# Kernel tuning notes

Measured on AMD Instinct MI355X. Metric: run time of the kernel, lower is better.

The kernel has to match this reference:

```python
import jax, jax.numpy as jnp
import numpy as np

NUM_SAMPLES = 512
FG_FRACTION = 0.25
MAX_POS = int(NUM_SAMPLES * FG_FRACTION)  # 128
THRESHOLDS = np.array([0.0, 0.5, 0.5], dtype=np.float32)
INDICATORS = np.array([-3, -1, -2, 1], dtype=np.int32)


def _make_boxes(key, shape, scale):
    # random valid boxes: sorted corner pairs in [0, scale)
    y = jnp.sort(jax.random.uniform(key, shape[:-1] + (2,)) * scale, axis=-1)
    x = jnp.sort(jax.random.uniform(jax.random.fold_in(key, 1), shape[:-1] + (2,)) * scale, axis=-1)
    return jnp.stack([y[..., 0], x[..., 0], y[..., 1], x[..., 1]], axis=-1)


def setup_inputs() -> dict:
    key = jax.random.key(0)
    k1, k2, k3, k4 = jax.random.split(key, 4)
    B, N, M = 32, 8000, 256
    boxes = _make_boxes(k1, (B, N, 4), 1024.0)
    gt_boxes = _make_boxes(k2, (B, M, 4), 1024.0)
    # pad last quarter of gt entries with -1 (invalid)
    valid = (jnp.arange(M) < (3 * M) // 4)[None, :, None]
    gt_boxes = jnp.where(valid, gt_boxes, -jnp.ones_like(gt_boxes))
    gt_classes = jax.random.randint(k3, (B, M), 1, 91, dtype=jnp.int32)
    gt_classes = jnp.where(valid[..., 0], gt_classes, -1)
    rand = jax.random.uniform(k4, (B, N + M))
    return {"boxes": boxes, "gt_boxes": gt_boxes, "gt_classes": gt_classes, "rand": rand}


def _pairwise_iou(b1, b2):
    # b1: [B,N,4], b2: [B,M,4] in (ymin,xmin,ymax,xmax) -> [B,N,M]
    ymin1, xmin1, ymax1, xmax1 = jnp.split(b1, 4, axis=-1)  # each [B,N,1]
    ymin2, xmin2, ymax2, xmax2 = (t[..., 0] for t in jnp.split(b2, 4, axis=-1))  # [B,M]
    ih = jnp.clip(jnp.minimum(ymax1, ymax2[:, None, :]) - jnp.maximum(ymin1, ymin2[:, None, :]), 0.0)
    iw = jnp.clip(jnp.minimum(xmax1, xmax2[:, None, :]) - jnp.maximum(xmin1, xmin2[:, None, :]), 0.0)
    inter = ih * iw
    a1 = (ymax1 - ymin1) * (xmax1 - xmin1)          # [B,N,1]
    a2 = (ymax2 - ymin2) * (xmax2 - xmin2)          # [B,M]
    union = a1 + a2[:, None, :] - inter
    return jnp.where(union > 0, inter / union, 0.0)


def _ranks_desc(score):
    order = jnp.argsort(-score)
    return jnp.zeros_like(order).at[order].set(jnp.arange(score.shape[0]))


def _sample_one(pos, neg, ign, rand):
    cand = (pos | neg) & ~ign
    pos_c = pos & cand
    neg_c = neg & cand
    pos_rank = _ranks_desc(jnp.where(pos_c, rand, -1.0))
    pos_sel = pos_c & (pos_rank < MAX_POS)
    neg_needed = NUM_SAMPLES - jnp.sum(pos_sel)
    neg_rank = _ranks_desc(jnp.where(neg_c, rand, -1.0))
    neg_sel = neg_c & (neg_rank < neg_needed)
    indicator = (pos_sel | neg_sel).astype(jnp.int32)
    _, idx = jax.lax.top_k(indicator, NUM_SAMPLES)  # selected first, ties by lowest index
    return idx


def _gather(t, idx):
    # t: [B,L,C], idx: [B,K] -> [B,K,C]
    return jnp.take_along_axis(t, idx[..., None], axis=1)


def reference(boxes, gt_boxes, gt_classes, rand):
    gt_boxes = gt_boxes.astype(boxes.dtype)
    boxes = jnp.concatenate([boxes, gt_boxes], axis=1)  # mix_gt_boxes
    boxes_invalid = jnp.max(boxes, axis=-1) < 0.0       # [B,L]
    gt_invalid = jnp.max(gt_boxes, axis=-1) < 0.0       # [B,M]
    sim = _pairwise_iou(boxes, gt_boxes)                # [B,L,M]
    sim = jnp.where(boxes_invalid[:, :, None] | gt_invalid[:, None, :], -1.0, sim)

    matched_vals = jnp.max(sim, axis=-1)                # [B,L]
    matched_gt_indices = jnp.argmax(sim, axis=-1).astype(jnp.int32)
    bucket = jnp.searchsorted(jnp.asarray(THRESHOLDS), matched_vals, side='right')
    match_indicators = jnp.asarray(INDICATORS)[bucket]  # [B,L]

    positive = match_indicators >= 0
    negative = match_indicators == -1
    ignored = match_indicators == -2
    invalid = match_indicators == -3
    background = negative | invalid                     # [B,L]

    matched_gt_classes = _gather(gt_classes[..., None], matched_gt_indices)[..., 0]
    matched_gt_classes = jnp.where(background, 0, matched_gt_classes)
    matched_gt_boxes = _gather(gt_boxes, matched_gt_indices)
    matched_gt_boxes = jnp.where(background[..., None], 0.0, matched_gt_boxes)
    matched_gt_indices = jnp.where(background, -1, matched_gt_indices)

    indices = jax.vmap(_sample_one)(positive, negative, ignored, rand)  # [B,K]
    rois = _gather(boxes, indices)
    sampled_gt_boxes = _gather(matched_gt_boxes, indices)
    sampled_gt_classes = _gather(matched_gt_classes[..., None], indices)[..., 0]
    sampled_gt_indices = _gather(matched_gt_indices[..., None], indices)[..., 0]
    return rois, sampled_gt_boxes, sampled_gt_classes, sampled_gt_indices
```

## Files before the change

kernel.cpp:

```cpp
#include <hip/hip_runtime.h>
#include <stdint.h>

#define BB 32
#define NN 8000
#define MM 256
#define LL (NN + MM)
#define NSAMP 512
#define MAXPOS 128
#define T2 1024
#define CH ((LL + T2 - 1) / T2)
#define SPLIT 4
#define MSUB (MM / SPLIT)

__device__ __forceinline__ void opaquef(float& x) { asm("" : "+v"(x)); }

__device__ __noinline__ int serial_argmax(const float4 bx, const float a1,
                                          const float4* s_gt, const float* s_a2)
{
    float qb = -1.0f; int bi = 0;
    for (int m = 0; m < MSUB; ++m) {
        float4 g = s_gt[m];
        float ih = fmaxf(fminf(bx.z, g.z) - fmaxf(bx.x, g.x), 0.0f);
        float iw = fmaxf(fminf(bx.w, g.w) - fmaxf(bx.y, g.y), 0.0f);
        float inter = ih * iw; opaquef(inter);
        float uni = (a1 + s_a2[m]) - inter;
        float q = (uni > 0.0f) ? (inter / uni) : 0.0f;
        if (q > qb) { qb = q; bi = m; }
    }
    return bi;
}

__device__ __forceinline__ uint32_t approx_key(const float4 bx, float a1,
                                               const float4 g, float a2, int m)
{
    float ih = fmaxf(fminf(bx.z, g.z) - fmaxf(bx.x, g.x), 0.0f);
    float iw = fmaxf(fminf(bx.w, g.w) - fmaxf(bx.y, g.y), 0.0f);
    float inter = ih * iw;
    float s = fmaxf(a1 + a2, 1e-30f);
    float u = inter * __builtin_amdgcn_rcpf(s);
    return (__float_as_uint(u) & 0xFFFFFFC0u) | (uint32_t)(63 - m);
}

template<bool FUSED>
__global__ __launch_bounds__(256) void match_split_kernel(
    const float* __restrict__ boxes, const float* __restrict__ gt,
    void* __restrict__ outp)
{
    __shared__ float4 s_gt[MSUB];
    __shared__ float  s_a2[MSUB];
    const int b = blockIdx.y, sp = blockIdx.z, tid = threadIdx.x;
    if (tid < MSUB) {
        float4 v = ((const float4*)(gt + ((size_t)b * MM + sp * MSUB) * 4))[tid];
        s_gt[tid] = v;
        s_a2[tid] = (v.z - v.x) * (v.w - v.y);
    }
    __syncthreads();
    const int l0 = blockIdx.x * 512 + tid * 2;
    if (l0 >= LL) return;
    const int l1 = l0 + 1;
    const bool v1 = (l1 < LL);
    const int l1c = v1 ? l1 : l0;

    const float4* bb4 = (const float4*)(boxes + (size_t)b * NN * 4);
    const float4* gb4 = (const float4*)(gt + (size_t)b * MM * 4);
    float4 bx0 = (l0 < NN) ? bb4[l0] : gb4[l0 - NN];
    float4 bx1 = (l1c < NN) ? bb4[l1c] : gb4[l1c - NN];
    float a10 = (bx0.z - bx0.x) * (bx0.w - bx0.y); opaquef(a10);
    float a11 = (bx1.z - bx1.x) * (bx1.w - bx1.y); opaquef(a11);

    uint32_t best0 = 0, sec0 = 0, best1 = 0, sec1 = 0;
    #pragma unroll 8
    for (int m = 0; m < MSUB; ++m) {
        const float4 g = s_gt[m];
        const float a2 = s_a2[m];
        {
            uint32_t key = approx_key(bx0, a10, g, a2, m);
            uint32_t old = best0;
            best0 = max(old, key);
            sec0  = max(sec0, min(old, key));
        }
        {
            uint32_t key = approx_key(bx1, a11, g, a2, m);
            uint32_t old = best1;
            best1 = max(old, key);
            sec1  = max(sec1, min(old, key));
        }
    }

    bool redo0 = ((best0 & ~63u) != 0u) &&
                 (((best0 & ~63u) - (sec0 & ~63u)) <= 64u);
    bool redo1 = v1 && ((best1 & ~63u) != 0u) &&
                 (((best1 & ~63u) - (sec1 & ~63u)) <= 64u);
    if (__any(redo0 || redo1)) {
        if (redo0) {
            int mW = serial_argmax(bx0, a10, s_gt, s_a2);
            best0 = approx_key(bx0, a10, s_gt[mW], s_a2[mW], mW);
        }
        if (redo1) {
            int mW = serial_argmax(bx1, a11, s_gt, s_a2);
            best1 = approx_key(bx1, a11, s_gt[mW], s_a2[mW], mW);
        }
    }
    if (FUSED) {
        uint32_t* keys = (uint32_t*)outp;
        keys[((size_t)b * LL + l0) * SPLIT + sp] = best0;
        if (v1) keys[((size_t)b * LL + l1) * SPLIT + sp] = best1;
    } else {
        uint8_t* pidx = (uint8_t*)outp;
        pidx[((size_t)b * LL + l0) * SPLIT + sp] = (uint8_t)(63 - (best0 & 63u));
        if (v1) pidx[((size_t)b * LL + l1) * SPLIT + sp] = (uint8_t)(63 - (best1 & 63u));
    }
}

__global__ __launch_bounds__(256) void merge_kernel(
    const float* __restrict__ boxes, const float* __restrict__ gt,
    const uint8_t* __restrict__ pidx, uint16_t* __restrict__ packed)
{
    const int b = blockIdx.y;
    const int l = blockIdx.x * 256 + threadIdx.x;
    if (l >= LL) return;
    float4 bx = (l < NN) ? ((const float4*)(boxes + (size_t)b * NN * 4))[l]
                         : ((const float4*)(gt + (size_t)b * MM * 4))[l - NN];
    int cls, bidx = 0;
    if (fmaxf(fmaxf(bx.x, bx.y), fmaxf(bx.z, bx.w)) < 0.0f) {
        cls = 2;
    } else {
        float a1 = (bx.z - bx.x) * (bx.w - bx.y); opaquef(a1);
        float qb = -1.0f;
        const uint32_t pv = *(const uint32_t*)&pidx[((size_t)b * LL + l) * SPLIT];
        #pragma unroll
        for (int sp = 0; sp < SPLIT; ++sp) {
            const int m = sp * MSUB + (int)((pv >> (8 * sp)) & 0xFFu);
            float4 g = ((const float4*)(gt + (size_t)b * MM * 4))[m];
            float a2 = (g.z - g.x) * (g.w - g.y); opaquef(a2);
            float ih = fmaxf(fminf(bx.z, g.z) - fmaxf(bx.x, g.x), 0.0f);
            float iw = fmaxf(fminf(bx.w, g.w) - fmaxf(bx.y, g.y), 0.0f);
            float inter = ih * iw; opaquef(inter);
            float uni = (a1 + a2) - inter;
            float q = (uni > 0.0f) ? (inter / uni) : 0.0f;
            if (q > qb) { qb = q; bidx = m; }
        }
        cls = (qb >= 0.5f) ? 1 : 0;
    }
    packed[(size_t)b * LL + l] = (uint16_t)(cls | (bidx << 2));
}

__device__ __forceinline__ int block_exscan_fast(int v, int* wt, int tid)
{
    const int lane = tid & 63, w = tid >> 6;
    int x = v;
    #pragma unroll
    for (int off = 1; off < 64; off <<= 1) {
        int y = __shfl_up(x, off);
        if (lane >= off) x += y;
    }
    if (lane == 63) wt[w] = x;
    __syncthreads();
    if (tid < 64) {
        int t = (tid < 16) ? wt[tid] : 0;
        #pragma unroll
        for (int off = 1; off < 16; off <<= 1) {
            int y = __shfl_up(t, off);
            if (tid >= off) t += y;
        }
        if (tid < 16) wt[tid] = t;
    }
    __syncthreads();
    return ((w > 0) ? wt[w - 1] : 0) + x - v;
}

__device__ __forceinline__ int block_exscan_seg4(int v, int* wt, int tid)
{
    const int lane = tid & 63, w = tid >> 6;
    int x = v;
    #pragma unroll
    for (int off = 1; off < 64; off <<= 1) {
        int y = __shfl_up(x, off);
        if (lane >= off) x += y;
    }
    if (lane == 63) wt[w] = x;
    __syncthreads();
    if (tid < 16) {
        int t = wt[tid];
        #pragma unroll
        for (int off = 1; off < 4; off <<= 1) {
            int y = __shfl_up(t, off);
            if ((tid & 3) >= off) t += y;
        }
        wt[tid] = t;
    }
    __syncthreads();
    return (((w & 3) > 0) ? wt[w - 1] : 0) + x - v;
}

template<bool FUSED>
__global__ __launch_bounds__(T2) void sample_kernel(
    const float* __restrict__ boxes, const float* __restrict__ gt,
    const int* __restrict__ gtc, const float* __restrict__ rnd,
    const void* __restrict__ matchp, float* __restrict__ out)
{
    __shared__ uint32_t s_key[LL];
    __shared__ uint16_t s_pk[LL];
    __shared__ int s_hist[512];
    __shared__ int s_warp[16];
    __shared__ int s_idx[NSAMP];
    __shared__ int s_sb[8];
    const int b = blockIdx.x, tid = threadIdx.x, lane = tid & 63;
    const float4* bb4 = (const float4*)(boxes + (size_t)b * NN * 4);
    const float4* gb4 = (const float4*)(gt + (size_t)b * MM * 4);

    if (tid == 0) s_sb[0] = 0;
    __syncthreads();

    int loc = 0;
    for (int l = tid; l < LL; l += T2) {
        s_key[l] = __float_as_uint(rnd[(size_t)b * LL + l]);
        int cls, midx;
        if (FUSED) {
            const uint4 kv = ((const uint4*)matchp)[(size_t)b * LL + l];
            float4 bx = (l < NN) ? bb4[l] : gb4[l - NN];
            if (fmaxf(fmaxf(bx.x, bx.y), fmaxf(bx.z, bx.w)) < 0.0f) {
                cls = 2; midx = 0;
            } else {
                uint32_t best = kv.x; int bsp = 0;
                if (kv.y > best) { best = kv.y; bsp = 1; }
                if (kv.z > best) { best = kv.z; bsp = 2; }
                if (kv.w > best) { best = kv.w; bsp = 3; }
                const uint32_t bt = best & ~63u;
                const uint32_t s0 = (bsp == 0) ? 0u : (kv.x & ~63u);
                const uint32_t s1 = (bsp == 1) ? 0u : (kv.y & ~63u);
                const uint32_t s2 = (bsp == 2) ? 0u : (kv.z & ~63u);
                const uint32_t s3 = (bsp == 3) ? 0u : (kv.w & ~63u);
                const uint32_t sec = max(max(s0, s1), max(s2, s3));
                float a1 = (bx.z - bx.x) * (bx.w - bx.y); opaquef(a1);
                if ((bt != 0u) && (bt - sec) <= 64u) {
                    float qb = -1.0f; midx = 0;
                    #pragma unroll
                    for (int sp = 0; sp < SPLIT; ++sp) {
                        const uint32_t k = (sp == 0) ? kv.x : (sp == 1) ? kv.y
                                         : (sp == 2) ? kv.z : kv.w;
                        const int m = sp * MSUB + (63 - (int)(k & 63u));
                        float4 g = gb4[m];
                        float a2 = (g.z - g.x) * (g.w - g.y); opaquef(a2);
                        float ih = fmaxf(fminf(bx.z, g.z) - fmaxf(bx.x, g.x), 0.0f);
                        float iw = fmaxf(fminf(bx.w, g.w) - fmaxf(bx.y, g.y), 0.0f);
                        float inter = ih * iw; opaquef(inter);
                        float uni = (a1 + a2) - inter;
                        float q = (uni > 0.0f) ? (inter / uni) : 0.0f;
                        if (q > qb) { qb = q; midx = m; }
                    }
                    cls = (qb >= 0.5f) ? 1 : 0;
                } else {
                    midx = bsp * MSUB + (63 - (int)(best & 63u));
                    float4 g = gb4[midx];
                    float a2 = (g.z - g.x) * (g.w - g.y); opaquef(a2);
                    float ih = fmaxf(fminf(bx.z, g.z) - fmaxf(bx.x, g.x), 0.0f);
                    float iw = fmaxf(fminf(bx.w, g.w) - fmaxf(bx.y, g.y), 0.0f);
                    float inter = ih * iw; opaquef(inter);
                    float uni = (a1 + a2) - inter;
                    float q = (uni > 0.0f) ? (inter / uni) : 0.0f;
                    cls = (q >= 0.5f) ? 1 : 0;
                }
            }
        } else {
            const uint16_t p = ((const uint16_t*)matchp)[(size_t)b * LL + l];
            cls = p & 3; midx = (p >> 2) & 0xFF;
        }
        s_pk[l] = (uint16_t)(cls | (midx << 2));
        loc += (cls == 0) ? 1 : ((cls == 1) ? 0x10000 : 0);
    }
    #pragma unroll
    for (int off = 32; off; off >>= 1) loc += __shfl_xor(loc, off);
    if (lane == 0) atomicAdd(&s_sb[0], loc);
    __syncthreads();
    const int Nn = s_sb[0] & 0xFFFF, P = s_sb[0] >> 16;

    const int posK = (P < MAXPOS) ? P : MAXPOS;
    const int negK = NSAMP - posK;
    const bool negRad = (Nn > negK);
    const bool posRad = (P > MAXPOS);

    uint32_t prefix0 = 0, prefix1 = 0;
    int rem0 = negK, rem1 = MAXPOS;
    if (negRad || posRad) {
        for (int round = 0; round < 4; ++round) {
            const int shift = 24 - 8 * round;
            if (tid < 512) s_hist[tid] = 0;
            __syncthreads();
            const uint32_t pmask = (round == 0) ? 0u : (0xFFFFFFFFu << (shift + 8));
            for (int l = tid; l < LL; l += T2) {
                const uint32_t k = s_key[l];
                const int c = s_pk[l] & 3;
                bool doit = (c == 0) ? (negRad && ((k & pmask) == prefix0))
                          : (c == 1) ? (posRad && ((k & pmask) == prefix1))
                          : false;
                if (doit) atomicAdd(&s_hist[(c << 8) | ((k >> shift) & 255)], 1);
            }
            __syncthreads();
            int h = 0;
            if (tid < 512) h = s_hist[(tid & 0x100) | (255 - (tid & 255))];
            const int above = block_exscan_seg4(h, s_warp, tid);
            if (tid < 512) {
                const int c = tid >> 8;
                const int rem = c ? rem1 : rem0;
                const bool act = c ? posRad : negRad;
                if (act && above < rem && above + h >= rem) {
                    s_sb[4 + c * 2] = 255 - (tid & 255);
                    s_sb[5 + c * 2] = above;
                }
            }
            __syncthreads();
            if (negRad) { prefix0 |= ((uint32_t)s_sb[4]) << shift; rem0 -= s_sb[5]; }
            if (posRad) { prefix1 |= ((uint32_t)s_sb[6]) << shift; rem1 -= s_sb[7]; }
            __syncthreads();
        }
    }
    const uint32_t thr0 = negRad ? prefix0 : 0u;  const int r0 = negRad ? rem0 : LL;
    const uint32_t thr1 = posRad ? prefix1 : 0u;  const int r1 = posRad ? rem1 : LL;

    const int lo = tid * CH, hi = (lo + CH < LL) ? (lo + CH) : LL;
    int nt = 0;
    for (int l = lo; l < hi; ++l) {
        const int c = s_pk[l] & 3;
        const uint32_t k = s_key[l];
        if (c == 0) { if (k == thr0) nt += 1; }
        else if (c == 1) { if (k == thr1) nt += 0x10000; }
    }
    const int basep = block_exscan_fast(nt, s_warp, tid);
    int base0 = basep & 0xFFFF, base1 = basep >> 16;
    for (int l = lo; l < hi; ++l) {
        const int c = s_pk[l] & 3;
        if (c > 1) continue;
        const uint32_t k = s_key[l];
        const uint32_t thr = c ? thr1 : thr0;
        bool sel = (k > thr);
        if (k == thr) {
            if (c == 0) { sel = (base0 < r0); ++base0; }
            else        { sel = (base1 < r1); ++base1; }
        }
        if (sel) s_pk[l] |= 0x8000;
    }
    __syncthreads();

    int cnt = 0;
    for (int l = lo; l < hi; ++l) cnt += (s_pk[l] & 0x8000) ? 1 : 0x10000;
    const int pb = block_exscan_fast(cnt, s_warp, tid);
    const int S = s_warp[15] & 0xFFFF;
    int bs = pb & 0xFFFF, bu = (pb >> 16) + S;
    for (int l = lo; l < hi; ++l) {
        if (s_pk[l] & 0x8000) { if (bs < NSAMP) s_idx[bs] = l; ++bs; }
        else                  { if (bu < NSAMP) s_idx[bu] = l; ++bu; }
    }
    __syncthreads();

    if (tid < NSAMP) {
        const int l = s_idx[tid];
        float4 bx = (l < NN) ? bb4[l] : gb4[l - NN];
        const int p = s_pk[l];
        const int c = p & 3, mi = (p >> 2) & 0xFF;
        const bool bg = (c != 1);
        float4 gb = make_float4(0.f, 0.f, 0.f, 0.f);
        int cl = 0, si = -1;
        if (!bg) {
            gb = gb4[mi];
            cl = gtc[(size_t)b * MM + mi];
            si = mi;
        }
        const size_t rk = (size_t)b * NSAMP + tid;
        ((float4*)out)[rk] = bx;
        ((float4*)(out + (size_t)BB * NSAMP * 4))[rk] = gb;
        out[(size_t)2 * BB * NSAMP * 4 + rk] = (float)cl;
        out[(size_t)2 * BB * NSAMP * 4 + (size_t)BB * NSAMP + rk] = (float)si;
    }
}

extern "C" void kernel_launch(void* const* d_in, const int* in_sizes, int n_in,
                              void* d_out, int out_size, void* d_ws, size_t ws_size,
                              hipStream_t stream)
{
    const float* boxes = (const float*)d_in[0];
    const float* gt    = (const float*)d_in[1];
    const int*   gtc   = (const int*)  d_in[2];
    const float* rnd   = (const float*)d_in[3];
    float* out = (float*)d_out;

    dim3 g1((LL + 511) / 512, BB, SPLIT);
    const size_t need = (size_t)BB * LL * SPLIT * sizeof(uint32_t);
    if (ws_size >= need) {
        match_split_kernel<true><<<g1, 256, 0, stream>>>(boxes, gt, d_ws);
        sample_kernel<true><<<BB, T2, 0, stream>>>(boxes, gt, gtc, rnd, d_ws, out);
    } else {
        uint8_t*  pidx   = (uint8_t*)d_ws;
        uint16_t* packed = (uint16_t*)((char*)d_ws + (size_t)BB * LL * SPLIT);
        match_split_kernel<false><<<g1, 256, 0, stream>>>(boxes, gt, pidx);
        dim3 g2((LL + 255) / 256, BB);
        merge_kernel<<<g2, 256, 0, stream>>>(boxes, gt, pidx, packed);
        sample_kernel<false><<<BB, T2, 0, stream>>>(boxes, gt, gtc, rnd, packed, out);
    }
}
```

Measured before the change: 75.49 us.

## Compact invalid GT boxes out of match loop and split key merge into separate kernel

The match kernel now compacts each 64-wide GT slice in shared memory so that only valid (non-padded) GT boxes are scanned. It keeps the original index in a per-entry key suffix so tie-breaking is preserved. The 4-way key merge and exact IoU recheck move out of the 32-block sample kernel into a new wide merge kernel, which writes a packed class/index in place into the key buffer. This spreads the serial per-row merge work across many blocks but adds a third kernel launch and an extra global round trip.

Measured after the change: 70.97 us. -6.0%, faster.

```diff
diff --git a/kernel.cpp b/kernel.cpp
--- a/kernel.cpp
+++ b/kernel.cpp
@@ -14,11 +14,24 @@
 
 __device__ __forceinline__ void opaquef(float& x) { asm("" : "+v"(x)); }
 
+__device__ __forceinline__ uint32_t approx_key(const float4 bx, float a1,
+                                               const float4 g, float a2,
+                                               uint32_t klo)
+{
+    float ih = fmaxf(fminf(bx.z, g.z) - fmaxf(bx.x, g.x), 0.0f);
+    float iw = fmaxf(fminf(bx.w, g.w) - fmaxf(bx.y, g.y), 0.0f);
+    float inter = ih * iw;
+    float s = fmaxf(a1 + a2, 1e-30f);
+    float u = inter * __builtin_amdgcn_rcpf(s);
+    return (__float_as_uint(u) & 0xFFFFFFC0u) | klo;
+}
+
 __device__ __noinline__ int serial_argmax(const float4 bx, const float a1,
-                                          const float4* s_gt, const float* s_a2)
+                                          const float4* s_gt, const float* s_a2,
+                                          int nv)
 {
     float qb = -1.0f; int bi = 0;
-    for (int m = 0; m < MSUB; ++m) {
+    for (int m = 0; m < nv; ++m) {
         float4 g = s_gt[m];
         float ih = fmaxf(fminf(bx.z, g.z) - fmaxf(bx.x, g.x), 0.0f);
         float iw = fmaxf(fminf(bx.w, g.w) - fmaxf(bx.y, g.y), 0.0f);
@@ -30,29 +43,26 @@
     return bi;
 }
 
-__device__ __forceinline__ uint32_t approx_key(const float4 bx, float a1,
-                                               const float4 g, float a2, int m)
-{
-    float ih = fmaxf(fminf(bx.z, g.z) - fmaxf(bx.x, g.x), 0.0f);
-    float iw = fmaxf(fminf(bx.w, g.w) - fmaxf(bx.y, g.y), 0.0f);
-    float inter = ih * iw;
-    float s = fmaxf(a1 + a2, 1e-30f);
-    float u = inter * __builtin_amdgcn_rcpf(s);
-    return (__float_as_uint(u) & 0xFFFFFFC0u) | (uint32_t)(63 - m);
-}
-
-template<bool FUSED>
 __global__ __launch_bounds__(256) void match_split_kernel(
     const float* __restrict__ boxes, const float* __restrict__ gt,
-    void* __restrict__ outp)
+    uint32_t* __restrict__ keys)
 {
     __shared__ float4 s_gt[MSUB];
     __shared__ float  s_a2[MSUB];
+    __shared__ uint32_t s_klo[MSUB];
+    __shared__ int s_nv;
     const int b = blockIdx.y, sp = blockIdx.z, tid = threadIdx.x;
     if (tid < MSUB) {
         float4 v = ((const float4*)(gt + ((size_t)b * MM + sp * MSUB) * 4))[tid];
-        s_gt[tid] = v;
-        s_a2[tid] = (v.z - v.x) * (v.w - v.y);
+        bool valid = !(fmaxf(fmaxf(v.x, v.y), fmaxf(v.z, v.w)) < 0.0f);
+        uint64_t mk = __ballot(valid);
+        int pos = __popcll(mk & ((1ull << tid) - 1));
+        if (valid) {
+            s_gt[pos] = v;
+            s_a2[pos] = (v.z - v.x) * (v.w - v.y);
+            s_klo[pos] = (uint32_t)(63 - tid);
+        }
+        if (tid == 0) s_nv = (int)__popcll(mk);
     }
     __syncthreads();
     const int l0 = blockIdx.x * 512 + tid * 2;
@@ -60,6 +70,7 @@
     const int l1 = l0 + 1;
     const bool v1 = (l1 < LL);
     const int l1c = v1 ? l1 : l0;
+    const int nv = s_nv;
 
     const float4* bb4 = (const float4*)(boxes + (size_t)b * NN * 4);
     const float4* gb4 = (const float4*)(gt + (size_t)b * MM * 4);
@@ -69,18 +80,19 @@
     float a11 = (bx1.z - bx1.x) * (bx1.w - bx1.y); opaquef(a11);
 
     uint32_t best0 = 0, sec0 = 0, best1 = 0, sec1 = 0;
-    #pragma unroll 8
-    for (int m = 0; m < MSUB; ++m) {
+    #pragma unroll 4
+    for (int m = 0; m < nv; ++m) {
         const float4 g = s_gt[m];
         const float a2 = s_a2[m];
+        const uint32_t klo = s_klo[m];
         {
-            uint32_t key = approx_key(bx0, a10, g, a2, m);
+            uint32_t key = approx_key(bx0, a10, g, a2, klo);
             uint32_t old = best0;
             best0 = max(old, key);
             sec0  = max(sec0, min(old, key));
         }
         {
-            uint32_t key = approx_key(bx1, a11, g, a2, m);
+            uint32_t key = approx_key(bx1, a11, g, a2, klo);
             uint32_t old = best1;
             best1 = max(old, key);
             sec1  = max(sec1, min(old, key));
@@ -93,56 +105,74 @@
                  (((best1 & ~63u) - (sec1 & ~63u)) <= 64u);
     if (__any(redo0 || redo1)) {
         if (redo0) {
-            int mW = serial_argmax(bx0, a10, s_gt, s_a2);
-            best0 = approx_key(bx0, a10, s_gt[mW], s_a2[mW], mW);
+            int w = serial_argmax(bx0, a10, s_gt, s_a2, nv);
+            best0 = approx_key(bx0, a10, s_gt[w], s_a2[w], s_klo[w]);
         }
         if (redo1) {
-            int mW = serial_argmax(bx1, a11, s_gt, s_a2);
-            best1 = approx_key(bx1, a11, s_gt[mW], s_a2[mW], mW);
-        }
-    }
-    if (FUSED) {
-        uint32_t* keys = (uint32_t*)outp;
-        keys[((size_t)b * LL + l0) * SPLIT + sp] = best0;
-        if (v1) keys[((size_t)b * LL + l1) * SPLIT + sp] = best1;
-    } else {
-        uint8_t* pidx = (uint8_t*)outp;
-        pidx[((size_t)b * LL + l0) * SPLIT + sp] = (uint8_t)(63 - (best0 & 63u));
-        if (v1) pidx[((size_t)b * LL + l1) * SPLIT + sp] = (uint8_t)(63 - (best1 & 63u));
-    }
-}
-
-__global__ __launch_bounds__(256) void merge_kernel(
+            int w = serial_argmax(bx1, a11, s_gt, s_a2, nv);
+            best1 = approx_key(bx1, a11, s_gt[w], s_a2[w], s_klo[w]);
+        }
+    }
+    keys[((size_t)b * LL + l0) * SPLIT + sp] = best0;
+    if (v1) keys[((size_t)b * LL + l1) * SPLIT + sp] = best1;
+}
+
+__global__ __launch_bounds__(256) void merge2_kernel(
     const float* __restrict__ boxes, const float* __restrict__ gt,
-    const uint8_t* __restrict__ pidx, uint16_t* __restrict__ packed)
+    uint32_t* __restrict__ keys)
 {
     const int b = blockIdx.y;
     const int l = blockIdx.x * 256 + threadIdx.x;
     if (l >= LL) return;
-    float4 bx = (l < NN) ? ((const float4*)(boxes + (size_t)b * NN * 4))[l]
-                         : ((const float4*)(gt + (size_t)b * MM * 4))[l - NN];
-    int cls, bidx = 0;
+    const float4* bb4 = (const float4*)(boxes + (size_t)b * NN * 4);
+    const float4* gb4 = (const float4*)(gt + (size_t)b * MM * 4);
+    const uint4 kv = ((const uint4*)keys)[(size_t)b * LL + l];
+    float4 bx = (l < NN) ? bb4[l] : gb4[l - NN];
+    int cls, midx = 0;
     if (fmaxf(fmaxf(bx.x, bx.y), fmaxf(bx.z, bx.w)) < 0.0f) {
         cls = 2;
     } else {
+        uint32_t best = kv.x; int bsp = 0;
+        if (kv.y > best) { best = kv.y; bsp = 1; }
+        if (kv.z > best) { best = kv.z; bsp = 2; }
+        if (kv.w > best) { best = kv.w; bsp = 3; }
+        const uint32_t bt = best & ~63u;
+        const uint32_t s0 = (bsp == 0) ? 0u : (kv.x & ~63u);
+        const uint32_t s1 = (bsp == 1) ? 0u : (kv.y & ~63u);
+        const uint32_t s2 = (bsp == 2) ? 0u : (kv.z & ~63u);
+        const uint32_t s3 = (bsp == 3) ? 0u : (kv.w & ~63u);
+        const uint32_t sec = max(max(s0, s1), max(s2, s3));
         float a1 = (bx.z - bx.x) * (bx.w - bx.y); opaquef(a1);
-        float qb = -1.0f;
-        const uint32_t pv = *(const uint32_t*)&pidx[((size_t)b * LL + l) * SPLIT];
-        #pragma unroll
-        for (int sp = 0; sp < SPLIT; ++sp) {
-            const int m = sp * MSUB + (int)((pv >> (8 * sp)) & 0xFFu);
-            float4 g = ((const float4*)(gt + (size_t)b * MM * 4))[m];
+        if ((bt != 0u) && (bt - sec) <= 64u) {
+            float qb = -1.0f; midx = 0;
+            #pragma unroll
+            for (int sp = 0; sp < SPLIT; ++sp) {
+                const uint32_t k = (sp == 0) ? kv.x : (sp == 1) ? kv.y
+                                 : (sp == 2) ? kv.z : kv.w;
+                const int m = sp * MSUB + (63 - (int)(k & 63u));
+                float4 g = gb4[m];
+                float a2 = (g.z - g.x) * (g.w - g.y); opaquef(a2);
+                float ih = fmaxf(fminf(bx.z, g.z) - fmaxf(bx.x, g.x), 0.0f);
+                float iw = fmaxf(fminf(bx.w, g.w) - fmaxf(bx.y, g.y), 0.0f);
+                float inter = ih * iw; opaquef(inter);
+                float uni = (a1 + a2) - inter;
+                float q = (uni > 0.0f) ? (inter / uni) : 0.0f;
+                if (q > qb) { qb = q; midx = m; }
+            }
+            cls = (qb >= 0.5f) ? 1 : 0;
+        } else {
+            midx = bsp * MSUB + (63 - (int)(best & 63u));
+            float4 g = gb4[midx];
             float a2 = (g.z - g.x) * (g.w - g.y); opaquef(a2);
             float ih = fmaxf(fminf(bx.z, g.z) - fmaxf(bx.x, g.x), 0.0f);
             float iw = fmaxf(fminf(bx.w, g.w) - fmaxf(bx.y, g.y), 0.0f);
             float inter = ih * iw; opaquef(inter);
             float uni = (a1 + a2) - inter;
             float q = (uni > 0.0f) ? (inter / uni) : 0.0f;
-            if (q > qb) { qb = q; bidx = m; }
-        }
-        cls = (qb >= 0.5f) ? 1 : 0;
-    }
-    packed[(size_t)b * LL + l] = (uint16_t)(cls | (bidx << 2));
+            cls = (q >= 0.5f) ? 1 : 0;
+        }
+    }
+    ((uint16_t*)keys)[((size_t)b * LL + l) * 8] = (uint16_t)(cls | (midx << 2));
 }
 
 __device__ __forceinline__ int block_exscan_fast(int v, int* wt, int tid)
@@ -193,11 +223,10 @@
     return (((w & 3) > 0) ? wt[w - 1] : 0) + x - v;
 }
 
-template<bool FUSED>
 __global__ __launch_bounds__(T2) void sample_kernel(
     const float* __restrict__ boxes, const float* __restrict__ gt,
     const int* __restrict__ gtc, const float* __restrict__ rnd,
-    const void* __restrict__ matchp, float* __restrict__ out)
+    const uint32_t* __restrict__ keys, float* __restrict__ out)
 {
     __shared__ uint32_t s_key[LL];
     __shared__ uint16_t s_pk[LL];
@@ -215,59 +244,10 @@
     int loc = 0;
     for (int l = tid; l < LL; l += T2) {
         s_key[l] = __float_as_uint(rnd[(size_t)b * LL + l]);
-        int cls, midx;
-        if (FUSED) {
-            const uint4 kv = ((const uint4*)matchp)[(size_t)b * LL + l];
-            float4 bx = (l < NN) ? bb4[l] : gb4[l - NN];
-            if (fmaxf(fmaxf(bx.x, bx.y), fmaxf(bx.z, bx.w)) < 0.0f) {
-                cls = 2; midx = 0;
-            } else {
-                uint32_t best = kv.x; int bsp = 0;
-                if (kv.y > best) { best = kv.y; bsp = 1; }
-                if (kv.z > best) { best = kv.z; bsp = 2; }
-                if (kv.w > best) { best = kv.w; bsp = 3; }
-                const uint32_t bt = best & ~63u;
-                const uint32_t s0 = (bsp == 0) ? 0u : (kv.x & ~63u);
-                const uint32_t s1 = (bsp == 1) ? 0u : (kv.y & ~63u);
-                const uint32_t s2 = (bsp == 2) ? 0u : (kv.z & ~63u);
-                const uint32_t s3 = (bsp == 3) ? 0u : (kv.w & ~63u);
-                const uint32_t sec = max(max(s0, s1), max(s2, s3));
-                float a1 = (bx.z - bx.x) * (bx.w - bx.y); opaquef(a1);
-                if ((bt != 0u) && (bt - sec) <= 64u) {
-                    float qb = -1.0f; midx = 0;
-                    #pragma unroll
-                    for (int sp = 0; sp < SPLIT; ++sp) {
-                        const uint32_t k = (sp == 0) ? kv.x : (sp == 1) ? kv.y
-                                         : (sp == 2) ? kv.z : kv.w;
-                        const int m = sp * MSUB + (63 - (int)(k & 63u));
-                        float4 g = gb4[m];
-                        float a2 = (g.z - g.x) * (g.w - g.y); opaquef(a2);
-                        float ih = fmaxf(fminf(bx.z, g.z) - fmaxf(bx.x, g.x), 0.0f);
-                        float iw = fmaxf(fminf(bx.w, g.w) - fmaxf(bx.y, g.y), 0.0f);
-                        float inter = ih * iw; opaquef(inter);
-                        float uni = (a1 + a2) - inter;
-                        float q = (uni > 0.0f) ? (inter / uni) : 0.0f;
-                        if (q > qb) { qb = q; midx = m; }
-                    }
-                    cls = (qb >= 0.5f) ? 1 : 0;
-                } else {
-                    midx = bsp * MSUB + (63 - (int)(best & 63u));
-                    float4 g = gb4[midx];
-                    float a2 = (g.z - g.x) * (g.w - g.y); opaquef(a2);
-                    float ih = fmaxf(fminf(bx.z, g.z) - fmaxf(bx.x, g.x), 0.0f);
-                    float iw = fmaxf(fminf(bx.w, g.w) - fmaxf(bx.y, g.y), 0.0f);
-                    float inter = ih * iw; opaquef(inter);
-                    float uni = (a1 + a2) - inter;
-                    float q = (uni > 0.0f) ? (inter / uni) : 0.0f;
-                    cls = (q >= 0.5f) ? 1 : 0;
-                }
-            }
-        } else {
-            const uint16_t p = ((const uint16_t*)matchp)[(size_t)b * LL + l];
-            cls = p & 3; midx = (p >> 2) & 0xFF;
-        }
-        s_pk[l] = (uint16_t)(cls | (midx << 2));
-        loc += (cls == 0) ? 1 : ((cls == 1) ? 0x10000 : 0);
+        uint16_t p = ((const uint16_t*)keys)[((size_t)b * LL + l) * 8];
+        s_pk[l] = p;
+        int c = p & 3;
+        loc += (c == 0) ? 1 : ((c == 1) ? 0x10000 : 0);
     }
     #pragma unroll
     for (int off = 32; off; off >>= 1) loc += __shfl_xor(loc, off);
@@ -383,18 +363,11 @@
     const int*   gtc   = (const int*)  d_in[2];
     const float* rnd   = (const float*)d_in[3];
     float* out = (float*)d_out;
+    uint32_t* keys = (uint32_t*)d_ws;
 
     dim3 g1((LL + 511) / 512, BB, SPLIT);
-    const size_t need = (size_t)BB * LL * SPLIT * sizeof(uint32_t);
-    if (ws_size >= need) {
-        match_split_kernel<true><<<g1, 256, 0, stream>>>(boxes, gt, d_ws);
-        sample_kernel<true><<<BB, T2, 0, stream>>>(boxes, gt, gtc, rnd, d_ws, out);
-    } else {
-        uint8_t*  pidx   = (uint8_t*)d_ws;
-        uint16_t* packed = (uint16_t*)((char*)d_ws + (size_t)BB * LL * SPLIT);
-        match_split_kernel<false><<<g1, 256, 0, stream>>>(boxes, gt, pidx);
-        dim3 g2((LL + 255) / 256, BB);
-        merge_kernel<<<g2, 256, 0, stream>>>(boxes, gt, pidx, packed);
-        sample_kernel<false><<<BB, T2, 0, stream>>>(boxes, gt, gtc, rnd, packed, out);
-    }
-}
+    match_split_kernel<<<g1, 256, 0, stream>>>(boxes, gt, keys);
+    dim3 g2((LL + 255) / 256, BB);
+    merge2_kernel<<<g2, 256, 0, stream>>>(boxes, gt, keys);
+    sample_kernel<<<BB, T2, 0, stream>>>(boxes, gt, gtc, rnd, keys, out);
+}
```
